# Optimization experiments

Hardware: AMD Instinct MI355X
Metric: run time of the kernel (lower is better)

## Reference

```python
import jax, jax.numpy as jnp
import numpy as np

BATCH = 16      # self.batch_size
EPS = 1e-5      # BatchNorm2d default eps


def setup_inputs() -> dict:
    key = jax.random.key(0)
    ks = jax.random.split(key, 8)
    inp = {
        # mailbox['agg_feat']: [total_nodes = B*npoints, K, C_in] = [16384, 64, 67]
        'agg_feat': jax.random.normal(ks[0], (16384, 64, 67), jnp.float32),
        # layer 0: Conv2d(67, 64, 1) + BN(64)
        'w0': jax.random.normal(ks[1], (64, 67), jnp.float32) * 0.1,
        'b0': jnp.zeros((64,), jnp.float32),
        'g0': jnp.ones((64,), jnp.float32),
        'be0': jnp.zeros((64,), jnp.float32),
        # layer 1: Conv2d(64, 64, 1) + BN(64)
        'w1': jax.random.normal(ks[2], (64, 64), jnp.float32) * 0.1,
        'b1': jnp.zeros((64,), jnp.float32),
        'g1': jnp.ones((64,), jnp.float32),
        'be1': jnp.zeros((64,), jnp.float32),
        # layer 2: Conv2d(64, 128, 1) + BN(128)
        'w2': jax.random.normal(ks[3], (128, 64), jnp.float32) * 0.1,
        'b2': jnp.zeros((128,), jnp.float32),
        'g2': jnp.ones((128,), jnp.float32),
        'be2': jnp.zeros((128,), jnp.float32),
    }
    return inp


def _conv_bn_relu(h, w, b, g, be):
    # 1x1 Conv2d on NCHW: contraction over input channels only
    h = jnp.einsum('oc,bcnk->bonk', w, h) + b[None, :, None, None]
    # BatchNorm2d in training mode: biased batch stats over (B, N, K) per channel
    mean = jnp.mean(h, axis=(0, 2, 3), keepdims=True)
    var = jnp.mean(jnp.square(h - mean), axis=(0, 2, 3), keepdims=True)
    h = (h - mean) * jax.lax.rsqrt(var + EPS)
    h = h * g[None, :, None, None] + be[None, :, None, None]
    return jax.nn.relu(h)


def reference(agg_feat, w0, b0, g0, be0, w1, b1, g1, be1, w2, b2, g2, be2):
    total, K, C = agg_feat.shape
    npoints = total // BATCH
    # [total, K, C] -> [B, npoints, K, C] -> [B, C, npoints, K]
    h = agg_feat.reshape(BATCH, npoints, K, C).transpose(0, 3, 1, 2)
    for w, b, g, be in ((w0, b0, g0, be0), (w1, b1, g1, be1), (w2, b2, g2, be2)):
        h = _conv_bn_relu(h, w, b, g, be)
    # max over neighbor axis K -> [B, C_out, npoints]
    h = jnp.max(h, axis=3)
    feat_dim = h.shape[1]
    # [B, C_out, npoints] -> [B, npoints, C_out] -> [B*npoints, C_out]
    return h.transpose(0, 2, 1).reshape(-1, feat_dim)
```

## Files before the change

### kernel.cpp

```cpp
#include <hip/hip_runtime.h>
#include <hip/hip_bf16.h>

#define ROWS  16384
#define PTOT  1048576
#define NTOTF 1048576.0f
#define EPSF  1e-5f
#define NREP  16

typedef __attribute__((ext_vector_type(8))) short short8;
typedef __attribute__((ext_vector_type(4))) float floatx4;
typedef float f32x4 __attribute__((ext_vector_type(4)));
typedef f32x4 f32x4u __attribute__((aligned(4)));

union FU { float f; unsigned int u; };

__device__ __forceinline__ float bfbits2f(unsigned short s) {
    FU fu; fu.u = ((unsigned int)s) << 16; return fu.f;
}
__device__ __forceinline__ unsigned short f2bfbits(float x) {
    FU fu; fu.f = x;
    unsigned int r = fu.u + 0x7FFFu + ((fu.u >> 16) & 1u);
    return (unsigned short)(r >> 16);
}
__device__ __forceinline__ float relu_f(float x) { return x > 0.f ? x : 0.f; }

__global__ __launch_bounds__(256) void k_conv0(
    const float* __restrict__ X, const float* __restrict__ w0,
    const float* __restrict__ b0, unsigned short* __restrict__ H,
    float* __restrict__ stats)
{
    __shared__ float sred[64], s2red[64];
    const int tid  = threadIdx.x;
    const int lane = tid & 63;
    const int wid  = tid >> 6;
    const int ln15 = lane & 15;
    const int quad = lane >> 4;
    const int pbase = blockIdx.x * 256 + wid * 64;

    if (tid < 64) { sred[tid] = 0.f; s2red[tid] = 0.f; }
    __syncthreads();

    short8 afr[4][3];
    floatx4 bias[4];
#pragma unroll
    for (int mt = 0; mt < 4; ++mt) {
        const float* wr = w0 + (size_t)(mt * 16 + ln15) * 67;
#pragma unroll
        for (int kh = 0; kh < 2; ++kh) {
            f32x4u wa = *reinterpret_cast<const f32x4u*>(wr + kh * 32 + quad * 8);
            f32x4u wb = *reinterpret_cast<const f32x4u*>(wr + kh * 32 + quad * 8 + 4);
            short8 v;
#pragma unroll
            for (int j = 0; j < 4; ++j) { v[j] = (short)f2bfbits(wa[j]); v[4 + j] = (short)f2bfbits(wb[j]); }
            afr[mt][kh] = v;
        }
        short8 t = {0, 0, 0, 0, 0, 0, 0, 0};
        if (quad == 0) {
            f32x4u tv = *reinterpret_cast<const f32x4u*>(wr + 63);
            t[0] = (short)f2bfbits(tv[1]); t[1] = (short)f2bfbits(tv[2]); t[2] = (short)f2bfbits(tv[3]);
        }
        afr[mt][2] = t;
        bias[mt] = *reinterpret_cast<const floatx4*>(b0 + mt * 16 + quad * 4);
    }

    float s[4][4] = {}, s2[4][4] = {};
#pragma unroll 2
    for (int nt = 0; nt < 4; ++nt) {
        const int pos = pbase + nt * 16 + ln15;
        const float* xr = X + (size_t)pos * 67;
        short8 bf0, bf1, bft = {0, 0, 0, 0, 0, 0, 0, 0};
        {
            f32x4u xa = *reinterpret_cast<const f32x4u*>(xr + quad * 8);
            f32x4u xb = *reinterpret_cast<const f32x4u*>(xr + quad * 8 + 4);
            f32x4u xc = *reinterpret_cast<const f32x4u*>(xr + 32 + quad * 8);
            f32x4u xd = *reinterpret_cast<const f32x4u*>(xr + 32 + quad * 8 + 4);
#pragma unroll
            for (int j = 0; j < 4; ++j) {
                bf0[j] = (short)f2bfbits(xa[j]); bf0[4 + j] = (short)f2bfbits(xb[j]);
                bf1[j] = (short)f2bfbits(xc[j]); bf1[4 + j] = (short)f2bfbits(xd[j]);
            }
            if (quad == 0) {
                f32x4u tv = *reinterpret_cast<const f32x4u*>(xr + 63);
                bft[0] = (short)f2bfbits(tv[1]); bft[1] = (short)f2bfbits(tv[2]); bft[2] = (short)f2bfbits(tv[3]);
            }
        }
#pragma unroll
        for (int mt = 0; mt < 4; ++mt) {
            floatx4 c = {0.f, 0.f, 0.f, 0.f};
            c = __builtin_amdgcn_mfma_f32_16x16x32_bf16(afr[mt][0], bf0, c, 0, 0, 0);
            c = __builtin_amdgcn_mfma_f32_16x16x32_bf16(afr[mt][1], bf1, c, 0, 0, 0);
            c = __builtin_amdgcn_mfma_f32_16x16x32_bf16(afr[mt][2], bft, c, 0, 0, 0);
            uint2 o;
            float h0 = c[0] + bias[mt][0], h1 = c[1] + bias[mt][1];
            float h2 = c[2] + bias[mt][2], h3 = c[3] + bias[mt][3];
            s[mt][0] += h0; s2[mt][0] += h0 * h0;
            s[mt][1] += h1; s2[mt][1] += h1 * h1;
            s[mt][2] += h2; s2[mt][2] += h2 * h2;
            s[mt][3] += h3; s2[mt][3] += h3 * h3;
            o.x = (unsigned int)f2bfbits(h0) | ((unsigned int)f2bfbits(h1) << 16);
            o.y = (unsigned int)f2bfbits(h2) | ((unsigned int)f2bfbits(h3) << 16);
            *reinterpret_cast<uint2*>(&H[(size_t)pos * 64 + mt * 16 + quad * 4]) = o;
        }
    }
#pragma unroll
    for (int mt = 0; mt < 4; ++mt)
#pragma unroll
        for (int rg = 0; rg < 4; ++rg) {
            s[mt][rg]  += __shfl_xor(s[mt][rg], 1, 64);  s[mt][rg]  += __shfl_xor(s[mt][rg], 2, 64);
            s[mt][rg]  += __shfl_xor(s[mt][rg], 4, 64);  s[mt][rg]  += __shfl_xor(s[mt][rg], 8, 64);
            s2[mt][rg] += __shfl_xor(s2[mt][rg], 1, 64); s2[mt][rg] += __shfl_xor(s2[mt][rg], 2, 64);
            s2[mt][rg] += __shfl_xor(s2[mt][rg], 4, 64); s2[mt][rg] += __shfl_xor(s2[mt][rg], 8, 64);
        }
    if (ln15 == 0) {
#pragma unroll
        for (int mt = 0; mt < 4; ++mt)
#pragma unroll
            for (int rg = 0; rg < 4; ++rg) {
                atomicAdd(&sred[mt * 16 + quad * 4 + rg], s[mt][rg]);
                atomicAdd(&s2red[mt * 16 + quad * 4 + rg], s2[mt][rg]);
            }
    }
    __syncthreads();
    const int rep = (blockIdx.x & (NREP - 1)) * 512;
    if (tid < 64) {
        unsafeAtomicAdd(&stats[rep + tid], sred[tid]);
        unsafeAtomicAdd(&stats[rep + 64 + tid], s2red[tid]);
    }
}

__global__ __launch_bounds__(256) void k_conv1(
    const unsigned short* __restrict__ Hin, unsigned short* __restrict__ Hout,
    const float* __restrict__ w1, const float* __restrict__ b1,
    const float* __restrict__ g0, const float* __restrict__ be0,
    float* __restrict__ stats)
{
    __shared__ float als[64], bls[64], sred[64], s2red[64];
    const int tid  = threadIdx.x;
    const int lane = tid & 63;
    const int wid  = tid >> 6;
    const int ln15 = lane & 15;
    const int quad = lane >> 4;
    const int pbase = blockIdx.x * 256 + wid * 64;

    if (tid < 64) {
        float ssum = 0.f, qsum = 0.f;
#pragma unroll
        for (int r = 0; r < NREP; ++r) { ssum += stats[r * 512 + tid]; qsum += stats[r * 512 + 64 + tid]; }
        const float mean = ssum * (1.f / NTOTF);
        const float var  = qsum * (1.f / NTOTF) - mean * mean;
        const float a    = g0[tid] / sqrtf(var + EPSF);
        als[tid] = a; bls[tid] = be0[tid] - mean * a;
        sred[tid] = 0.f; s2red[tid] = 0.f;
    }
    __syncthreads();

    float alr[16], blr[16];
#pragma unroll
    for (int kh = 0; kh < 2; ++kh)
#pragma unroll
        for (int j = 0; j < 8; ++j) {
            alr[kh * 8 + j] = als[kh * 32 + quad * 8 + j];
            blr[kh * 8 + j] = bls[kh * 32 + quad * 8 + j];
        }

    short8 afr[4][2];
    floatx4 bias[4];
#pragma unroll
    for (int mt = 0; mt < 4; ++mt) {
        const float* wr = w1 + (size_t)(mt * 16 + ln15) * 64;
#pragma unroll
        for (int kh = 0; kh < 2; ++kh) {
            const float4* wp = (const float4*)(wr + kh * 32 + quad * 8);
            float4 wa = wp[0], wb = wp[1];
            short8 v;
            v[0] = (short)f2bfbits(wa.x); v[1] = (short)f2bfbits(wa.y);
            v[2] = (short)f2bfbits(wa.z); v[3] = (short)f2bfbits(wa.w);
            v[4] = (short)f2bfbits(wb.x); v[5] = (short)f2bfbits(wb.y);
            v[6] = (short)f2bfbits(wb.z); v[7] = (short)f2bfbits(wb.w);
            afr[mt][kh] = v;
        }
        bias[mt] = *reinterpret_cast<const floatx4*>(b1 + mt * 16 + quad * 4);
    }

    float s[4][4] = {}, s2[4][4] = {};
#pragma unroll 2
    for (int nt = 0; nt < 4; ++nt) {
        const int pos = pbase + nt * 16 + ln15;
        const short8 h0 = *reinterpret_cast<const short8*>(&Hin[(size_t)pos * 64 + quad * 8]);
        const short8 h1 = *reinterpret_cast<const short8*>(&Hin[(size_t)pos * 64 + 32 + quad * 8]);
        short8 bf0, bf1;
#pragma unroll
        for (int j = 0; j < 8; ++j) {
            bf0[j] = (short)f2bfbits(relu_f(alr[j] * bfbits2f((unsigned short)h0[j]) + blr[j]));
            bf1[j] = (short)f2bfbits(relu_f(alr[8 + j] * bfbits2f((unsigned short)h1[j]) + blr[8 + j]));
        }
#pragma unroll
        for (int mt = 0; mt < 4; ++mt) {
            floatx4 c = {0.f, 0.f, 0.f, 0.f};
            c = __builtin_amdgcn_mfma_f32_16x16x32_bf16(afr[mt][0], bf0, c, 0, 0, 0);
            c = __builtin_amdgcn_mfma_f32_16x16x32_bf16(afr[mt][1], bf1, c, 0, 0, 0);
            uint2 o;
            float h0v = c[0] + bias[mt][0], h1v = c[1] + bias[mt][1];
            float h2v = c[2] + bias[mt][2], h3v = c[3] + bias[mt][3];
            s[mt][0] += h0v; s2[mt][0] += h0v * h0v;
            s[mt][1] += h1v; s2[mt][1] += h1v * h1v;
            s[mt][2] += h2v; s2[mt][2] += h2v * h2v;
            s[mt][3] += h3v; s2[mt][3] += h3v * h3v;
            o.x = (unsigned int)f2bfbits(h0v) | ((unsigned int)f2bfbits(h1v) << 16);
            o.y = (unsigned int)f2bfbits(h2v) | ((unsigned int)f2bfbits(h3v) << 16);
            *reinterpret_cast<uint2*>(&Hout[(size_t)pos * 64 + mt * 16 + quad * 4]) = o;
        }
    }
#pragma unroll
    for (int mt = 0; mt < 4; ++mt)
#pragma unroll
        for (int rg = 0; rg < 4; ++rg) {
            s[mt][rg]  += __shfl_xor(s[mt][rg], 1, 64);  s[mt][rg]  += __shfl_xor(s[mt][rg], 2, 64);
            s[mt][rg]  += __shfl_xor(s[mt][rg], 4, 64);  s[mt][rg]  += __shfl_xor(s[mt][rg], 8, 64);
            s2[mt][rg] += __shfl_xor(s2[mt][rg], 1, 64); s2[mt][rg] += __shfl_xor(s2[mt][rg], 2, 64);
            s2[mt][rg] += __shfl_xor(s2[mt][rg], 4, 64); s2[mt][rg] += __shfl_xor(s2[mt][rg], 8, 64);
        }
    if (ln15 == 0) {
#pragma unroll
        for (int mt = 0; mt < 4; ++mt)
#pragma unroll
            for (int rg = 0; rg < 4; ++rg) {
                atomicAdd(&sred[mt * 16 + quad * 4 + rg], s[mt][rg]);
                atomicAdd(&s2red[mt * 16 + quad * 4 + rg], s2[mt][rg]);
            }
    }
    __syncthreads();
    const int rep = (blockIdx.x & (NREP - 1)) * 512;
    if (tid < 64) {
        unsafeAtomicAdd(&stats[rep + 128 + tid], sred[tid]);
        unsafeAtomicAdd(&stats[rep + 192 + tid], s2red[tid]);
    }
}

__global__ __launch_bounds__(256) void k_conv2(
    const unsigned short* __restrict__ H, const float* __restrict__ w2,
    const float* __restrict__ b2, const float* __restrict__ g1,
    const float* __restrict__ be1, float* __restrict__ rowmax,
    float* __restrict__ rowmin, float* __restrict__ stats)
{
    __shared__ float als[64], bls[64], sred[128], s2red[128];
    const int tid  = threadIdx.x;
    const int lane = tid & 63;
    const int wid  = tid >> 6;
    const int ln15 = lane & 15;
    const int quad = lane >> 4;
    const int r0   = blockIdx.x * 4;

    if (tid < 64) {
        float ssum = 0.f, qsum = 0.f;
#pragma unroll
        for (int r = 0; r < NREP; ++r) { ssum += stats[r * 512 + 128 + tid]; qsum += stats[r * 512 + 192 + tid]; }
        const float mean = ssum * (1.f / NTOTF);
        const float var  = qsum * (1.f / NTOTF) - mean * mean;
        const float a    = g1[tid] / sqrtf(var + EPSF);
        als[tid] = a; bls[tid] = be1[tid] - mean * a;
    }
    if (tid < 128) { sred[tid] = 0.f; s2red[tid] = 0.f; }
    __syncthreads();

    float alr[16], blr[16];
#pragma unroll
    for (int kh = 0; kh < 2; ++kh)
#pragma unroll
        for (int j = 0; j < 8; ++j) {
            alr[kh * 8 + j] = als[kh * 32 + quad * 8 + j];
            blr[kh * 8 + j] = bls[kh * 32 + quad * 8 + j];
        }

    const int chHalf = (wid & 1) * 64;
    short8 bfr[8];
    float bias[4];
#pragma unroll
    for (int nt = 0; nt < 4; ++nt) {
        const int n = chHalf + nt * 16 + ln15;
        bias[nt] = b2[n];
#pragma unroll
        for (int kh = 0; kh < 2; ++kh) {
            const float4* wp = (const float4*)&w2[(size_t)n * 64 + kh * 32 + quad * 8];
            float4 wa = wp[0], wb = wp[1];
            short8 v;
            v[0] = (short)f2bfbits(wa.x); v[1] = (short)f2bfbits(wa.y);
            v[2] = (short)f2bfbits(wa.z); v[3] = (short)f2bfbits(wa.w);
            v[4] = (short)f2bfbits(wb.x); v[5] = (short)f2bfbits(wb.y);
            v[6] = (short)f2bfbits(wb.z); v[7] = (short)f2bfbits(wb.w);
            bfr[nt * 2 + kh] = v;
        }
    }

    float s[4] = {0, 0, 0, 0}, s2[4] = {0, 0, 0, 0};
    for (int rr = 0; rr < 2; ++rr) {
        const int prow = r0 + (wid >> 1) * 2 + rr;
        float mx[4] = {-3.4e38f, -3.4e38f, -3.4e38f, -3.4e38f};
        float mn[4] = {3.4e38f, 3.4e38f, 3.4e38f, 3.4e38f};
#pragma unroll 2
        for (int mt = 0; mt < 4; ++mt) {
            const size_t rowb = (size_t)(prow * 64 + mt * 16 + ln15) * 64;
            const short8 h0 = *reinterpret_cast<const short8*>(&H[rowb + quad * 8]);
            const short8 h1 = *reinterpret_cast<const short8*>(&H[rowb + 32 + quad * 8]);
            short8 a0, a1;
#pragma unroll
            for (int j = 0; j < 8; ++j) {
                a0[j] = (short)f2bfbits(relu_f(alr[j] * bfbits2f((unsigned short)h0[j]) + blr[j]));
                a1[j] = (short)f2bfbits(relu_f(alr[8 + j] * bfbits2f((unsigned short)h1[j]) + blr[8 + j]));
            }
#pragma unroll
            for (int nt = 0; nt < 4; ++nt) {
                floatx4 a = {0.f, 0.f, 0.f, 0.f};
                a = __builtin_amdgcn_mfma_f32_16x16x32_bf16(a0, bfr[nt * 2 + 0], a, 0, 0, 0);
                a = __builtin_amdgcn_mfma_f32_16x16x32_bf16(a1, bfr[nt * 2 + 1], a, 0, 0, 0);
#pragma unroll
                for (int rg = 0; rg < 4; ++rg) {
                    const float h = a[rg] + bias[nt];
                    mx[nt] = fmaxf(mx[nt], h);
                    mn[nt] = fminf(mn[nt], h);
                    s[nt] += h; s2[nt] += h * h;
                }
            }
        }
#pragma unroll
        for (int nt = 0; nt < 4; ++nt) {
            mx[nt] = fmaxf(mx[nt], __shfl_xor(mx[nt], 16, 64));
            mx[nt] = fmaxf(mx[nt], __shfl_xor(mx[nt], 32, 64));
            mn[nt] = fminf(mn[nt], __shfl_xor(mn[nt], 16, 64));
            mn[nt] = fminf(mn[nt], __shfl_xor(mn[nt], 32, 64));
        }
        if (lane < 16) {
#pragma unroll
            for (int nt = 0; nt < 4; ++nt) {
                rowmax[(size_t)prow * 128 + chHalf + nt * 16 + lane] = mx[nt];
                rowmin[(size_t)prow * 128 + chHalf + nt * 16 + lane] = mn[nt];
            }
        }
    }
#pragma unroll
    for (int nt = 0; nt < 4; ++nt) {
        s[nt]  += __shfl_xor(s[nt], 16, 64);  s[nt]  += __shfl_xor(s[nt], 32, 64);
        s2[nt] += __shfl_xor(s2[nt], 16, 64); s2[nt] += __shfl_xor(s2[nt], 32, 64);
    }
    if (lane < 16) {
#pragma unroll
        for (int nt = 0; nt < 4; ++nt) {
            atomicAdd(&sred[chHalf + nt * 16 + ln15], s[nt]);
            atomicAdd(&s2red[chHalf + nt * 16 + ln15], s2[nt]);
        }
    }
    __syncthreads();
    const int rep = (blockIdx.x & (NREP - 1)) * 512;
    if (tid < 128) {
        unsafeAtomicAdd(&stats[rep + 256 + tid], sred[tid]);
        unsafeAtomicAdd(&stats[rep + 384 + tid], s2red[tid]);
    }
}

__global__ __launch_bounds__(256) void k_out(
    const float* __restrict__ rowmax, const float* __restrict__ rowmin,
    const float* __restrict__ g2, const float* __restrict__ be2,
    const float* __restrict__ stats, float* __restrict__ out)
{
    __shared__ float als[128], bls[128];
    const int tid = threadIdx.x;
    if (tid < 128) {
        float ssum = 0.f, qsum = 0.f;
#pragma unroll
        for (int r = 0; r < NREP; ++r) { ssum += stats[r * 512 + 256 + tid]; qsum += stats[r * 512 + 384 + tid]; }
        const float mean = ssum * (1.f / NTOTF);
        const float var  = qsum * (1.f / NTOTF) - mean * mean;
        const float a    = g2[tid] / sqrtf(var + EPSF);
        als[tid] = a; bls[tid] = be2[tid] - mean * a;
    }
    __syncthreads();
    const int idx = blockIdx.x * 256 + tid;
    const int o = idx & 127;
    const float a = als[o];
    const float v = (a > 0.f) ? rowmax[idx] : rowmin[idx];
    out[idx] = relu_f(a * v + bls[o]);
}

extern "C" void kernel_launch(void* const* d_in, const int* in_sizes, int n_in,
                              void* d_out, int out_size, void* d_ws, size_t ws_size,
                              hipStream_t stream)
{
    (void)in_sizes; (void)n_in; (void)out_size; (void)ws_size;
    const float* X   = (const float*)d_in[0];
    const float* w0  = (const float*)d_in[1];
    const float* b0  = (const float*)d_in[2];
    const float* g0  = (const float*)d_in[3];
    const float* be0 = (const float*)d_in[4];
    const float* w1  = (const float*)d_in[5];
    const float* b1  = (const float*)d_in[6];
    const float* g1  = (const float*)d_in[7];
    const float* be1 = (const float*)d_in[8];
    const float* w2  = (const float*)d_in[9];
    const float* b2  = (const float*)d_in[10];
    const float* g2  = (const float*)d_in[11];
    const float* be2 = (const float*)d_in[12];
    float* out = (float*)d_out;

    char* ws = (char*)d_ws;
    unsigned short* H = (unsigned short*)ws;
    float* rowmax = (float*)(ws + 134217728);
    float* rowmin = (float*)(ws + 134217728 + 8388608);
    float* stats  = (float*)(ws + 134217728 + 2 * 8388608);

    hipMemsetAsync(stats, 0, NREP * 512 * sizeof(float), stream);
    hipLaunchKernelGGL(k_conv0, dim3(PTOT / 256), dim3(256), 0, stream, X, w0, b0, H, stats);
    hipLaunchKernelGGL(k_conv1, dim3(PTOT / 256), dim3(256), 0, stream, H, H, w1, b1, g0, be0, stats);
    hipLaunchKernelGGL(k_conv2, dim3(ROWS / 4), dim3(256), 0, stream, H, w2, b2, g1, be1, rowmax, rowmin, stats);
    hipLaunchKernelGGL(k_out, dim3(ROWS * 128 / 256), dim3(256), 0, stream, rowmax, rowmin, g2, be2, stats, out);
}
```

Measured before the change: 600.5 us.

## Switch intermediates to fp16 with packed conversions and half2 BN/ReLU

Replaces the bf16 intermediate format and the software round-to-nearest conversions with fp16, using the hardware packed convert (cvt_pkrtz) and fp16 MFMA. The BatchNorm plus ReLU applied on load is done with packed half2 FMA and max, and the bias is folded into the MFMA accumulator init. This cuts the VALU work spent on bit-manipulation conversions and the per-element float normalization. In exchange it trades bf16 range for fp16 precision and uses round-toward-zero, with some risk of overflow or precision differences in the intermediates and the BN scaling done in half.

```diff
diff --git a/kernel.cpp b/kernel.cpp
--- a/kernel.cpp
+++ b/kernel.cpp
@@ -1,5 +1,4 @@
 #include <hip/hip_runtime.h>
-#include <hip/hip_bf16.h>
 
 #define ROWS  16384
 #define PTOT  1048576
@@ -7,26 +6,38 @@
 #define EPSF  1e-5f
 #define NREP  16
 
-typedef __attribute__((ext_vector_type(8))) short short8;
+typedef _Float16 half8  __attribute__((ext_vector_type(8)));
+typedef _Float16 half2v __attribute__((ext_vector_type(2)));
+typedef __fp16   fp16x2 __attribute__((ext_vector_type(2)));
 typedef __attribute__((ext_vector_type(4))) float floatx4;
 typedef float f32x4 __attribute__((ext_vector_type(4)));
 typedef f32x4 f32x4u __attribute__((aligned(4)));
 
-union FU { float f; unsigned int u; };
-
-__device__ __forceinline__ float bfbits2f(unsigned short s) {
-    FU fu; fu.u = ((unsigned int)s) << 16; return fu.f;
-}
-__device__ __forceinline__ unsigned short f2bfbits(float x) {
-    FU fu; fu.f = x;
-    unsigned int r = fu.u + 0x7FFFu + ((fu.u >> 16) & 1u);
-    return (unsigned short)(r >> 16);
+union H8 { half8 v8; half2v v2[4]; };
+union PK2 { fp16x2 p; half2v h; unsigned int u; };
+
+__device__ __forceinline__ half2v cvt2(float lo, float hi) {
+    PK2 k; k.p = __builtin_amdgcn_cvt_pkrtz(lo, hi); return k.h;
+}
+__device__ __forceinline__ unsigned int cvt2u(float lo, float hi) {
+    PK2 k; k.p = __builtin_amdgcn_cvt_pkrtz(lo, hi); return k.u;
 }
 __device__ __forceinline__ float relu_f(float x) { return x > 0.f ? x : 0.f; }
+
+__device__ __forceinline__ half8 h8zero() {
+    half8 z = {(_Float16)0.f, (_Float16)0.f, (_Float16)0.f, (_Float16)0.f,
+               (_Float16)0.f, (_Float16)0.f, (_Float16)0.f, (_Float16)0.f};
+    return z;
+}
+
+__device__ __forceinline__ half2v bn2(half2v h, half2v a, half2v b) {
+    half2v z = {(_Float16)0.f, (_Float16)0.f};
+    return __builtin_elementwise_max((half2v)(h * a + b), z);
+}
 
 __global__ __launch_bounds__(256) void k_conv0(
     const float* __restrict__ X, const float* __restrict__ w0,
-    const float* __restrict__ b0, unsigned short* __restrict__ H,
+    const float* __restrict__ b0, _Float16* __restrict__ H,
     float* __restrict__ stats)
 {
     __shared__ float sred[64], s2red[64];
@@ -40,7 +51,7 @@
     if (tid < 64) { sred[tid] = 0.f; s2red[tid] = 0.f; }
     __syncthreads();
 
-    short8 afr[4][3];
+    half8 afr[4][3];
     floatx4 bias[4];
 #pragma unroll
     for (int mt = 0; mt < 4; ++mt) {
@@ -49,17 +60,20 @@
         for (int kh = 0; kh < 2; ++kh) {
             f32x4u wa = *reinterpret_cast<const f32x4u*>(wr + kh * 32 + quad * 8);
             f32x4u wb = *reinterpret_cast<const f32x4u*>(wr + kh * 32 + quad * 8 + 4);
-            short8 v;
-#pragma unroll
-            for (int j = 0; j < 4; ++j) { v[j] = (short)f2bfbits(wa[j]); v[4 + j] = (short)f2bfbits(wb[j]); }
-            afr[mt][kh] = v;
-        }
-        short8 t = {0, 0, 0, 0, 0, 0, 0, 0};
+            H8 t;
+            t.v2[0] = cvt2(wa[0], wa[1]);
+            t.v2[1] = cvt2(wa[2], wa[3]);
+            t.v2[2] = cvt2(wb[0], wb[1]);
+            t.v2[3] = cvt2(wb[2], wb[3]);
+            afr[mt][kh] = t.v8;
+        }
+        H8 t; t.v8 = h8zero();
         if (quad == 0) {
             f32x4u tv = *reinterpret_cast<const f32x4u*>(wr + 63);
-            t[0] = (short)f2bfbits(tv[1]); t[1] = (short)f2bfbits(tv[2]); t[2] = (short)f2bfbits(tv[3]);
-        }
-        afr[mt][2] = t;
+            t.v2[0] = cvt2(tv[1], tv[2]);
+            t.v2[1] = cvt2(tv[3], 0.f);
+        }
+        afr[mt][2] = t.v8;
         bias[mt] = *reinterpret_cast<const floatx4*>(b0 + mt * 16 + quad * 4);
     }
 
@@ -68,37 +82,40 @@
     for (int nt = 0; nt < 4; ++nt) {
         const int pos = pbase + nt * 16 + ln15;
         const float* xr = X + (size_t)pos * 67;
-        short8 bf0, bf1, bft = {0, 0, 0, 0, 0, 0, 0, 0};
+        H8 B0, B1, BT;
         {
             f32x4u xa = *reinterpret_cast<const f32x4u*>(xr + quad * 8);
             f32x4u xb = *reinterpret_cast<const f32x4u*>(xr + quad * 8 + 4);
             f32x4u xc = *reinterpret_cast<const f32x4u*>(xr + 32 + quad * 8);
             f32x4u xd = *reinterpret_cast<const f32x4u*>(xr + 32 + quad * 8 + 4);
-#pragma unroll
-            for (int j = 0; j < 4; ++j) {
-                bf0[j] = (short)f2bfbits(xa[j]); bf0[4 + j] = (short)f2bfbits(xb[j]);
-                bf1[j] = (short)f2bfbits(xc[j]); bf1[4 + j] = (short)f2bfbits(xd[j]);
-            }
+            B0.v2[0] = cvt2(xa[0], xa[1]);
+            B0.v2[1] = cvt2(xa[2], xa[3]);
+            B0.v2[2] = cvt2(xb[0], xb[1]);
+            B0.v2[3] = cvt2(xb[2], xb[3]);
+            B1.v2[0] = cvt2(xc[0], xc[1]);
+            B1.v2[1] = cvt2(xc[2], xc[3]);
+            B1.v2[2] = cvt2(xd[0], xd[1]);
+            B1.v2[3] = cvt2(xd[2], xd[3]);
+            BT.v8 = h8zero();
             if (quad == 0) {
                 f32x4u tv = *reinterpret_cast<const f32x4u*>(xr + 63);
-                bft[0] = (short)f2bfbits(tv[1]); bft[1] = (short)f2bfbits(tv[2]); bft[2] = (short)f2bfbits(tv[3]);
+                BT.v2[0] = cvt2(tv[1], tv[2]);
+                BT.v2[1] = cvt2(tv[3], 0.f);
             }
         }
 #pragma unroll
         for (int mt = 0; mt < 4; ++mt) {
-            floatx4 c = {0.f, 0.f, 0.f, 0.f};
-            c = __builtin_amdgcn_mfma_f32_16x16x32_bf16(afr[mt][0], bf0, c, 0, 0, 0);
-            c = __builtin_amdgcn_mfma_f32_16x16x32_bf16(afr[mt][1], bf1, c, 0, 0, 0);
-            c = __builtin_amdgcn_mfma_f32_16x16x32_bf16(afr[mt][2], bft, c, 0, 0, 0);
+            floatx4 c = bias[mt];
+            c = __builtin_amdgcn_mfma_f32_16x16x32_f16(afr[mt][0], B0.v8, c, 0, 0, 0);
+            c = __builtin_amdgcn_mfma_f32_16x16x32_f16(afr[mt][1], B1.v8, c, 0, 0, 0);
+            c = __builtin_amdgcn_mfma_f32_16x16x32_f16(afr[mt][2], BT.v8, c, 0, 0, 0);
+            s[mt][0] += c[0]; s2[mt][0] += c[0] * c[0];
+            s[mt][1] += c[1]; s2[mt][1] += c[1] * c[1];
+            s[mt][2] += c[2]; s2[mt][2] += c[2] * c[2];
+            s[mt][3] += c[3]; s2[mt][3] += c[3] * c[3];
             uint2 o;
-            float h0 = c[0] + bias[mt][0], h1 = c[1] + bias[mt][1];
-            float h2 = c[2] + bias[mt][2], h3 = c[3] + bias[mt][3];
-            s[mt][0] += h0; s2[mt][0] += h0 * h0;
-            s[mt][1] += h1; s2[mt][1] += h1 * h1;
-            s[mt][2] += h2; s2[mt][2] += h2 * h2;
-            s[mt][3] += h3; s2[mt][3] += h3 * h3;
-            o.x = (unsigned int)f2bfbits(h0) | ((unsigned int)f2bfbits(h1) << 16);
-            o.y = (unsigned int)f2bfbits(h2) | ((unsigned int)f2bfbits(h3) << 16);
+            o.x = cvt2u(c[0], c[1]);
+            o.y = cvt2u(c[2], c[3]);
             *reinterpret_cast<uint2*>(&H[(size_t)pos * 64 + mt * 16 + quad * 4]) = o;
         }
     }
@@ -129,7 +146,7 @@
 }
 
 __global__ __launch_bounds__(256) void k_conv1(
-    const unsigned short* __restrict__ Hin, unsigned short* __restrict__ Hout,
+    const _Float16* __restrict__ Hin, _Float16* __restrict__ Hout,
     const float* __restrict__ w1, const float* __restrict__ b1,
     const float* __restrict__ g0, const float* __restrict__ be0,
     float* __restrict__ stats)
@@ -154,30 +171,32 @@
     }
     __syncthreads();
 
-    float alr[16], blr[16];
+    half2v a2[8], b2[8];
 #pragma unroll
     for (int kh = 0; kh < 2; ++kh)
 #pragma unroll
-        for (int j = 0; j < 8; ++j) {
-            alr[kh * 8 + j] = als[kh * 32 + quad * 8 + j];
-            blr[kh * 8 + j] = bls[kh * 32 + quad * 8 + j];
-        }
-
-    short8 afr[4][2];
+        for (int j2 = 0; j2 < 4; ++j2) {
+            const int c0 = kh * 32 + quad * 8 + 2 * j2;
+            half2v av = {(_Float16)als[c0], (_Float16)als[c0 + 1]};
+            half2v bv = {(_Float16)bls[c0], (_Float16)bls[c0 + 1]};
+            a2[kh * 4 + j2] = av; b2[kh * 4 + j2] = bv;
+        }
+
+    half8 afr[4][2];
     floatx4 bias[4];
 #pragma unroll
     for (int mt = 0; mt < 4; ++mt) {
         const float* wr = w1 + (size_t)(mt * 16 + ln15) * 64;
 #pragma unroll
         for (int kh = 0; kh < 2; ++kh) {
-            const float4* wp = (const float4*)(wr + kh * 32 + quad * 8);
-            float4 wa = wp[0], wb = wp[1];
-            short8 v;
-            v[0] = (short)f2bfbits(wa.x); v[1] = (short)f2bfbits(wa.y);
-            v[2] = (short)f2bfbits(wa.z); v[3] = (short)f2bfbits(wa.w);
-            v[4] = (short)f2bfbits(wb.x); v[5] = (short)f2bfbits(wb.y);
-            v[6] = (short)f2bfbits(wb.z); v[7] = (short)f2bfbits(wb.w);
-            afr[mt][kh] = v;
+            f32x4 wa = *reinterpret_cast<const f32x4*>(wr + kh * 32 + quad * 8);
+            f32x4 wb = *reinterpret_cast<const f32x4*>(wr + kh * 32 + quad * 8 + 4);
+            H8 t;
+            t.v2[0] = cvt2(wa[0], wa[1]);
+            t.v2[1] = cvt2(wa[2], wa[3]);
+            t.v2[2] = cvt2(wb[0], wb[1]);
+            t.v2[3] = cvt2(wb[2], wb[3]);
+            afr[mt][kh] = t.v8;
         }
         bias[mt] = *reinterpret_cast<const floatx4*>(b1 + mt * 16 + quad * 4);
     }
@@ -186,28 +205,27 @@
 #pragma unroll 2
     for (int nt = 0; nt < 4; ++nt) {
         const int pos = pbase + nt * 16 + ln15;
-        const short8 h0 = *reinterpret_cast<const short8*>(&Hin[(size_t)pos * 64 + quad * 8]);
-        const short8 h1 = *reinterpret_cast<const short8*>(&Hin[(size_t)pos * 64 + 32 + quad * 8]);
-        short8 bf0, bf1;
-#pragma unroll
-        for (int j = 0; j < 8; ++j) {
-            bf0[j] = (short)f2bfbits(relu_f(alr[j] * bfbits2f((unsigned short)h0[j]) + blr[j]));
-            bf1[j] = (short)f2bfbits(relu_f(alr[8 + j] * bfbits2f((unsigned short)h1[j]) + blr[8 + j]));
+        H8 r0, r1;
+        r0.v8 = *reinterpret_cast<const half8*>(&Hin[(size_t)pos * 64 + quad * 8]);
+        r1.v8 = *reinterpret_cast<const half8*>(&Hin[(size_t)pos * 64 + 32 + quad * 8]);
+        H8 f0, f1;
+#pragma unroll
+        for (int j2 = 0; j2 < 4; ++j2) {
+            f0.v2[j2] = bn2(r0.v2[j2], a2[j2], b2[j2]);
+            f1.v2[j2] = bn2(r1.v2[j2], a2[4 + j2], b2[4 + j2]);
         }
 #pragma unroll
         for (int mt = 0; mt < 4; ++mt) {
-            floatx4 c = {0.f, 0.f, 0.f, 0.f};
-            c = __builtin_amdgcn_mfma_f32_16x16x32_bf16(afr[mt][0], bf0, c, 0, 0, 0);
-            c = __builtin_amdgcn_mfma_f32_16x16x32_bf16(afr[mt][1], bf1, c, 0, 0, 0);
+            floatx4 c = bias[mt];
+            c = __builtin_amdgcn_mfma_f32_16x16x32_f16(afr[mt][0], f0.v8, c, 0, 0, 0);
+            c = __builtin_amdgcn_mfma_f32_16x16x32_f16(afr[mt][1], f1.v8, c, 0, 0, 0);
+            s[mt][0] += c[0]; s2[mt][0] += c[0] * c[0];
+            s[mt][1] += c[1]; s2[mt][1] += c[1] * c[1];
+            s[mt][2] += c[2]; s2[mt][2] += c[2] * c[2];
+            s[mt][3] += c[3]; s2[mt][3] += c[3] * c[3];
             uint2 o;
-            float h0v = c[0] + bias[mt][0], h1v = c[1] + bias[mt][1];
-            float h2v = c[2] + bias[mt][2], h3v = c[3] + bias[mt][3];
-            s[mt][0] += h0v; s2[mt][0] += h0v * h0v;
-            s[mt][1] += h1v; s2[mt][1] += h1v * h1v;
-            s[mt][2] += h2v; s2[mt][2] += h2v * h2v;
-            s[mt][3] += h3v; s2[mt][3] += h3v * h3v;
-            o.x = (unsigned int)f2bfbits(h0v) | ((unsigned int)f2bfbits(h1v) << 16);
-            o.y = (unsigned int)f2bfbits(h2v) | ((unsigned int)f2bfbits(h3v) << 16);
+            o.x = cvt2u(c[0], c[1]);
+            o.y = cvt2u(c[2], c[3]);
             *reinterpret_cast<uint2*>(&Hout[(size_t)pos * 64 + mt * 16 + quad * 4]) = o;
         }
     }
@@ -238,8 +256,8 @@
 }
 
 __global__ __launch_bounds__(256) void k_conv2(
-    const unsigned short* __restrict__ H, const float* __restrict__ w2,
-    const float* __restrict__ b2, const float* __restrict__ g1,
+    const _Float16* __restrict__ H, const float* __restrict__ w2,
+    const float* __restrict__ b2c, const float* __restrict__ g1,
     const float* __restrict__ be1, float* __restrict__ rowmax,
     float* __restrict__ rowmin, float* __restrict__ stats)
 {
@@ -263,32 +281,34 @@
     if (tid < 128) { sred[tid] = 0.f; s2red[tid] = 0.f; }
     __syncthreads();
 
-    float alr[16], blr[16];
+    half2v a2[8], b2[8];
 #pragma unroll
     for (int kh = 0; kh < 2; ++kh)
 #pragma unroll
-        for (int j = 0; j < 8; ++j) {
-            alr[kh * 8 + j] = als[kh * 32 + quad * 8 + j];
-            blr[kh * 8 + j] = bls[kh * 32 + quad * 8 + j];
+        for (int j2 = 0; j2 < 4; ++j2) {
+            const int c0 = kh * 32 + quad * 8 + 2 * j2;
+            half2v av = {(_Float16)als[c0], (_Float16)als[c0 + 1]};
+            half2v bv = {(_Float16)bls[c0], (_Float16)bls[c0 + 1]};
+            a2[kh * 4 + j2] = av; b2[kh * 4 + j2] = bv;
         }
 
     const int chHalf = (wid & 1) * 64;
-    short8 bfr[8];
-    float bias[4];
+    half8 bfr[8];
+    float biasn[4];
 #pragma unroll
     for (int nt = 0; nt < 4; ++nt) {
         const int n = chHalf + nt * 16 + ln15;
-        bias[nt] = b2[n];
+        biasn[nt] = b2c[n];
 #pragma unroll
         for (int kh = 0; kh < 2; ++kh) {
-            const float4* wp = (const float4*)&w2[(size_t)n * 64 + kh * 32 + quad * 8];
-            float4 wa = wp[0], wb = wp[1];
-            short8 v;
-            v[0] = (short)f2bfbits(wa.x); v[1] = (short)f2bfbits(wa.y);
-            v[2] = (short)f2bfbits(wa.z); v[3] = (short)f2bfbits(wa.w);
-            v[4] = (short)f2bfbits(wb.x); v[5] = (short)f2bfbits(wb.y);
-            v[6] = (short)f2bfbits(wb.z); v[7] = (short)f2bfbits(wb.w);
-            bfr[nt * 2 + kh] = v;
+            f32x4 wa = *reinterpret_cast<const f32x4*>(&w2[(size_t)n * 64 + kh * 32 + quad * 8]);
+            f32x4 wb = *reinterpret_cast<const f32x4*>(&w2[(size_t)n * 64 + kh * 32 + quad * 8 + 4]);
+            H8 t;
+            t.v2[0] = cvt2(wa[0], wa[1]);
+            t.v2[1] = cvt2(wa[2], wa[3]);
+            t.v2[2] = cvt2(wb[0], wb[1]);
+            t.v2[3] = cvt2(wb[2], wb[3]);
+            bfr[nt * 2 + kh] = t.v8;
         }
     }
 
@@ -300,22 +320,23 @@
 #pragma unroll 2
         for (int mt = 0; mt < 4; ++mt) {
             const size_t rowb = (size_t)(prow * 64 + mt * 16 + ln15) * 64;
-            const short8 h0 = *reinterpret_cast<const short8*>(&H[rowb + quad * 8]);
-            const short8 h1 = *reinterpret_cast<const short8*>(&H[rowb + 32 + quad * 8]);
-            short8 a0, a1;
-#pragma unroll
-            for (int j = 0; j < 8; ++j) {
-                a0[j] = (short)f2bfbits(relu_f(alr[j] * bfbits2f((unsigned short)h0[j]) + blr[j]));
-                a1[j] = (short)f2bfbits(relu_f(alr[8 + j] * bfbits2f((unsigned short)h1[j]) + blr[8 + j]));
+            H8 r0f, r1f;
+            r0f.v8 = *reinterpret_cast<const half8*>(&H[rowb + quad * 8]);
+            r1f.v8 = *reinterpret_cast<const half8*>(&H[rowb + 32 + quad * 8]);
+            H8 f0, f1;
+#pragma unroll
+            for (int j2 = 0; j2 < 4; ++j2) {
+                f0.v2[j2] = bn2(r0f.v2[j2], a2[j2], b2[j2]);
+                f1.v2[j2] = bn2(r1f.v2[j2], a2[4 + j2], b2[4 + j2]);
             }
 #pragma unroll
             for (int nt = 0; nt < 4; ++nt) {
-                floatx4 a = {0.f, 0.f, 0.f, 0.f};
-                a = __builtin_amdgcn_mfma_f32_16x16x32_bf16(a0, bfr[nt * 2 + 0], a, 0, 0, 0);
-                a = __builtin_amdgcn_mfma_f32_16x16x32_bf16(a1, bfr[nt * 2 + 1], a, 0, 0, 0);
+                floatx4 a = {biasn[nt], biasn[nt], biasn[nt], biasn[nt]};
+                a = __builtin_amdgcn_mfma_f32_16x16x32_f16(f0.v8, bfr[nt * 2 + 0], a, 0, 0, 0);
+                a = __builtin_amdgcn_mfma_f32_16x16x32_f16(f1.v8, bfr[nt * 2 + 1], a, 0, 0, 0);
 #pragma unroll
                 for (int rg = 0; rg < 4; ++rg) {
-                    const float h = a[rg] + bias[nt];
+                    const float h = a[rg];
                     mx[nt] = fmaxf(mx[nt], h);
                     mn[nt] = fminf(mn[nt], h);
                     s[nt] += h; s2[nt] += h * h;
@@ -402,7 +423,7 @@
     float* out = (float*)d_out;
 
     char* ws = (char*)d_ws;
-    unsigned short* H = (unsigned short*)ws;
+    _Float16* H = (_Float16*)ws;
     float* rowmax = (float*)(ws + 134217728);
     float* rowmin = (float*)(ws + 134217728 + 8388608);
     float* stats  = (float*)(ws + 134217728 + 2 * 8388608);
```

Result: no change. 600.1 us (-0.1%).
